# Kernel optimization log

Hardware: AMD Instinct MI355X
Metric: run time of the kernel (lower is better)

The kernel has to match this reference:

```python
import jax, jax.numpy as jnp
import numpy as np

B, S, L, H, DH, D = 16, 512, 12, 12, 64, 768
M = L + 1  # embed + L mlp outputs


def setup_inputs() -> dict:
    key = jax.random.key(0)
    ks = jax.random.split(key, 8)
    return {
        "mlp_stack": jax.random.normal(ks[0], (B, S, M, D), jnp.float32),
        "attn_stack": jax.random.normal(ks[1], (B, S, L, H, DH), jnp.float32),
        "mlp_mask": jax.random.uniform(ks[2], (B, M), jnp.float32),
        "attn_mask": jax.random.uniform(ks[3], (B, L, H), jnp.float32),
        "modal_mlp": jax.random.normal(ks[4], (M, D), jnp.float32),
        "modal_attention": jax.random.normal(ks[5], (L, H, D), jnp.float32),
        "W_O": jax.random.normal(ks[6], (L, H, DH, D), jnp.float32) * 0.02,
        "post_bias": jax.random.normal(ks[7], (L, D), jnp.float32) * 0.02,
    }


def reference(mlp_stack, attn_stack, mlp_mask, attn_mask, modal_mlp,
              modal_attention, W_O, post_bias):
    # pruning_edge_mlp_hook_all_tokens at layer_no = n_layers (final hook path),
    # cache_compressed_attn=True, ablation_backward=False, non-parallel inference.
    # masked edge-weighted sum over cached mlp outputs: [B,1,M,1]*[B,S,M,D] -> sum over M
    out = jnp.einsum('bm,bsmd->bsd', mlp_mask, mlp_stack)
    # ablation (modal) term for pruned mlp edges: broadcasts over pos
    out = out + jnp.einsum('bm,md->bd', 1.0 - mlp_mask, modal_mlp)[:, None, :]
    # masked attention-head edges, recombined through W_O:
    # ([B,1,P,H,1]*[B,S,P,H,K]) einsum [P,H,K,D] -> [B,S,D]
    attn_term = jnp.einsum('bph,bsphk,phkd->bsd', attn_mask, attn_stack, W_O)
    out = out + attn_term + post_bias.sum(axis=0)
    # ablation (modal) term for pruned attention edges, summed over layer & head
    out = out + jnp.einsum('bph,phd->bd', 1.0 - attn_mask, modal_attention)[:, None, :]
    return out
```

## Files before the change

### kernel.cpp

```cpp
#include <hip/hip_runtime.h>


#define D_ 768
#define K_ 9216
#define ROWS_ 8192

typedef __attribute__((ext_vector_type(8))) short short8;
typedef __attribute__((ext_vector_type(4))) float f32x4;

typedef unsigned int __attribute__((address_space(1))) gu32;
typedef unsigned int __attribute__((address_space(3))) lu32;

__device__ __forceinline__ void async_copy16(const void* g, void* l) {
    __builtin_amdgcn_global_load_lds((const gu32*)g, (lu32*)l, 16, 0, 0);
}

__device__ __forceinline__ unsigned short f2bf(float f) {
    union { float f; unsigned u; } a; a.f = f;
    unsigned r = a.u + 0x7FFF + ((a.u >> 16) & 1);
    return (unsigned short)(r >> 16);
}

__global__ __launch_bounds__(256) void bias_kernel(
    const float* __restrict__ mlp_mask, const float* __restrict__ attn_mask,
    const float* __restrict__ modal_mlp, const float* __restrict__ modal_att,
    const float* __restrict__ post_bias, float* __restrict__ bias) {
    int b = blockIdx.x;
    for (int d = threadIdx.x; d < D_; d += 256) {
        float acc = 0.f;
        #pragma unroll
        for (int p = 0; p < 12; ++p) acc += post_bias[p * D_ + d];
        #pragma unroll
        for (int m = 0; m < 13; ++m)
            acc += (1.f - mlp_mask[b * 13 + m]) * modal_mlp[m * D_ + d];
        for (int ph = 0; ph < 144; ++ph)
            acc += (1.f - attn_mask[b * 144 + ph]) * modal_att[ph * D_ + d];
        bias[b * D_ + d] = acc;
    }
}

__global__ __launch_bounds__(256) void transpose_wo(
    const float* __restrict__ W, unsigned short* __restrict__ Bt) {
    __shared__ float tile[32][33];
    int n0 = blockIdx.x * 32;
    int k0 = blockIdx.y * 32;
    int tx = threadIdx.x & 31, ty = threadIdx.x >> 5;
    #pragma unroll
    for (int i = 0; i < 4; ++i)
        tile[ty + 8 * i][tx] = W[(k0 + ty + 8 * i) * D_ + n0 + tx];
    __syncthreads();
    #pragma unroll
    for (int i = 0; i < 4; ++i)
        Bt[(n0 + ty + 8 * i) * K_ + k0 + tx] = f2bf(tile[tx][ty + 8 * i]);
}

__global__ __launch_bounds__(256) void conv_attn(
    const float* __restrict__ attn_stack, const float* __restrict__ attn_mask,
    unsigned short* __restrict__ A) {
    int bid = blockIdx.x;
    int row = bid / 9;
    int k = ((bid - row * 9) * 256 + threadIdx.x) * 4;
    int b = row >> 9;
    float w = attn_mask[b * 144 + (k >> 6)];
    int i = row * K_ + k;
    float4 v = *(const float4*)&attn_stack[i];
    ushort4 o;
    o.x = f2bf(v.x * w); o.y = f2bf(v.y * w);
    o.z = f2bf(v.z * w); o.w = f2bf(v.w * w);
    *(ushort4*)&A[i] = o;
}

__global__ __launch_bounds__(256) void mlp_kernel(
    const float* __restrict__ mlp_stack, const float* __restrict__ mlp_mask,
    const float* __restrict__ bias, float* __restrict__ out) {
    int i4 = (blockIdx.x * 256 + threadIdx.x) * 4;
    int row = i4 / D_;
    int d = i4 - row * D_;
    int b = row >> 9;
    float4 acc = *(const float4*)&bias[b * D_ + d];
    const float* base = mlp_stack + (long)row * 13 * D_ + d;
    #pragma unroll
    for (int m = 0; m < 13; ++m) {
        float w = mlp_mask[b * 13 + m];
        float4 v = *(const float4*)&base[m * D_];
        acc.x += w * v.x; acc.y += w * v.y;
        acc.z += w * v.z; acc.w += w * v.w;
    }
    *(float4*)&out[i4] = acc;
}

__global__ __launch_bounds__(256) void gemm_attn(
    const short* __restrict__ A, const short* __restrict__ Bt,
    float* __restrict__ out) {
    __shared__ __align__(16) short As[128 * 32];
    __shared__ __align__(16) short Bs[128 * 32];

    const int tid = threadIdx.x;
    const int wave = tid >> 6, lane = tid & 63;
    const int row0 = blockIdx.x * 128;
    const int col0 = blockIdx.y * 128;
    const int wr = (wave >> 1) * 64;
    const int wc = (wave & 1) * 64;

    f32x4 acc[4][4] = {};

    const int rc = lane >> 2;
    const int x = lane & 3;
    const int g = x ^ ((rc >> 1) & 3);

    int a_off[2], b_off[2], lds_off[2];
    #pragma unroll
    for (int j = 0; j < 2; ++j) {
        int c = wave * 2 + j;
        a_off[j] = (row0 + c * 16 + rc) * K_ + g * 8;
        b_off[j] = (col0 + c * 16 + rc) * K_ + g * 8;
        lds_off[j] = c * 1024;
    }

    const int fr = lane & 15;
    const int q = lane >> 4;
    const int pos = q ^ ((fr >> 1) & 3);

    for (int k0 = 0; k0 < K_; k0 += 32) {
        __syncthreads();
        #pragma unroll
        for (int j = 0; j < 2; ++j) {
            async_copy16(A + a_off[j] + k0, (char*)As + lds_off[j]);
            async_copy16(Bt + b_off[j] + k0, (char*)Bs + lds_off[j]);
        }
        __syncthreads();

        short8 af[4], bf[4];
        #pragma unroll
        for (int i = 0; i < 4; ++i) {
            af[i] = *(const short8*)&As[(wr + i * 16 + fr) * 32 + pos * 8];
            bf[i] = *(const short8*)&Bs[(wc + i * 16 + fr) * 32 + pos * 8];
        }
        #pragma unroll
        for (int i = 0; i < 4; ++i)
            #pragma unroll
            for (int j = 0; j < 4; ++j)
                acc[i][j] = __builtin_amdgcn_mfma_f32_16x16x32_bf16(
                    af[i], bf[j], acc[i][j], 0, 0, 0);
    }

    #pragma unroll
    for (int i = 0; i < 4; ++i) {
        int m = row0 + wr + i * 16 + q * 4;
        #pragma unroll
        for (int j = 0; j < 4; ++j) {
            int n = col0 + wc + j * 16 + fr;
            float* p = out + m * D_ + n;
            #pragma unroll
            for (int r = 0; r < 4; ++r)
                p[r * D_] += acc[i][j][r];
        }
    }
}

extern "C" void kernel_launch(void* const* d_in, const int* in_sizes, int n_in,
                              void* d_out, int out_size, void* d_ws, size_t ws_size,
                              hipStream_t stream) {
    const float* mlp_stack  = (const float*)d_in[0];
    const float* attn_stack = (const float*)d_in[1];
    const float* mlp_mask   = (const float*)d_in[2];
    const float* attn_mask  = (const float*)d_in[3];
    const float* modal_mlp  = (const float*)d_in[4];
    const float* modal_att  = (const float*)d_in[5];
    const float* W_O        = (const float*)d_in[6];
    const float* post_bias  = (const float*)d_in[7];
    float* out = (float*)d_out;

    char* ws = (char*)d_ws;
    unsigned short* Abf = (unsigned short*)ws;
    unsigned short* Btb = (unsigned short*)(ws + 150994944);
    float* bias = (float*)(ws + 150994944 + 14155776);

    bias_kernel<<<16, 256, 0, stream>>>(mlp_mask, attn_mask, modal_mlp,
                                        modal_att, post_bias, bias);
    transpose_wo<<<dim3(24, 288), 256, 0, stream>>>(W_O, Btb);
    conv_attn<<<73728, 256, 0, stream>>>(attn_stack, attn_mask, Abf);
    mlp_kernel<<<6144, 256, 0, stream>>>(mlp_stack, mlp_mask, bias, out);
    gemm_attn<<<dim3(64, 6), 256, 0, stream>>>((const short*)Abf, (const short*)Btb, out);
}
```

Baseline: 898.7 us.

## Split-K the attention GEMM with atomic accumulation and widen conversion kernels

The bf16 attention GEMM is split four ways along K, growing the grid from 384 to 1536 blocks so more of the 256 CUs are busy. Partial tiles are combined into the output with float atomicAdd. The conversion kernel now handles 8 elements per thread with 16-byte stores, and the bias kernel is spread over more blocks. The cost is atomic write traffic to the output and a summation order that can differ from run to run.

```diff
diff --git a/kernel.cpp b/kernel.cpp
--- a/kernel.cpp
+++ b/kernel.cpp
@@ -4,8 +4,11 @@
 #define D_ 768
 #define K_ 9216
 #define ROWS_ 8192
+#define SPLITS 4
+#define KSPLIT (K_ / SPLITS)
 
 typedef __attribute__((ext_vector_type(8))) short short8;
+typedef __attribute__((ext_vector_type(8))) unsigned short ushort8;
 typedef __attribute__((ext_vector_type(4))) float f32x4;
 
 typedef unsigned int __attribute__((address_space(1))) gu32;
@@ -26,17 +29,17 @@
     const float* __restrict__ modal_mlp, const float* __restrict__ modal_att,
     const float* __restrict__ post_bias, float* __restrict__ bias) {
     int b = blockIdx.x;
-    for (int d = threadIdx.x; d < D_; d += 256) {
-        float acc = 0.f;
-        #pragma unroll
-        for (int p = 0; p < 12; ++p) acc += post_bias[p * D_ + d];
-        #pragma unroll
-        for (int m = 0; m < 13; ++m)
-            acc += (1.f - mlp_mask[b * 13 + m]) * modal_mlp[m * D_ + d];
-        for (int ph = 0; ph < 144; ++ph)
-            acc += (1.f - attn_mask[b * 144 + ph]) * modal_att[ph * D_ + d];
-        bias[b * D_ + d] = acc;
-    }
+    int d = blockIdx.y * 256 + threadIdx.x;
+    float acc = 0.f;
+    #pragma unroll
+    for (int p = 0; p < 12; ++p) acc += post_bias[p * D_ + d];
+    #pragma unroll
+    for (int m = 0; m < 13; ++m)
+        acc += (1.f - mlp_mask[b * 13 + m]) * modal_mlp[m * D_ + d];
+    #pragma unroll 16
+    for (int ph = 0; ph < 144; ++ph)
+        acc += (1.f - attn_mask[b * 144 + ph]) * modal_att[ph * D_ + d];
+    bias[b * D_ + d] = acc;
 }
 
 __global__ __launch_bounds__(256) void transpose_wo(
@@ -57,17 +60,19 @@
 __global__ __launch_bounds__(256) void conv_attn(
     const float* __restrict__ attn_stack, const float* __restrict__ attn_mask,
     unsigned short* __restrict__ A) {
-    int bid = blockIdx.x;
-    int row = bid / 9;
-    int k = ((bid - row * 9) * 256 + threadIdx.x) * 4;
+    int i = (blockIdx.x * 256 + threadIdx.x) * 8;
+    int row = i / K_;
+    int k = i - row * K_;
     int b = row >> 9;
     float w = attn_mask[b * 144 + (k >> 6)];
-    int i = row * K_ + k;
-    float4 v = *(const float4*)&attn_stack[i];
-    ushort4 o;
-    o.x = f2bf(v.x * w); o.y = f2bf(v.y * w);
-    o.z = f2bf(v.z * w); o.w = f2bf(v.w * w);
-    *(ushort4*)&A[i] = o;
+    float4 v0 = *(const float4*)&attn_stack[i];
+    float4 v1 = *(const float4*)&attn_stack[i + 4];
+    ushort8 o;
+    o[0] = f2bf(v0.x * w); o[1] = f2bf(v0.y * w);
+    o[2] = f2bf(v0.z * w); o[3] = f2bf(v0.w * w);
+    o[4] = f2bf(v1.x * w); o[5] = f2bf(v1.y * w);
+    o[6] = f2bf(v1.z * w); o[7] = f2bf(v1.w * w);
+    *(ushort8*)&A[i] = o;
 }
 
 __global__ __launch_bounds__(256) void mlp_kernel(
@@ -99,6 +104,7 @@
     const int wave = tid >> 6, lane = tid & 63;
     const int row0 = blockIdx.x * 128;
     const int col0 = blockIdx.y * 128;
+    const int kStart = blockIdx.z * KSPLIT;
     const int wr = (wave >> 1) * 64;
     const int wc = (wave & 1) * 64;
 
@@ -112,8 +118,8 @@
     #pragma unroll
     for (int j = 0; j < 2; ++j) {
         int c = wave * 2 + j;
-        a_off[j] = (row0 + c * 16 + rc) * K_ + g * 8;
-        b_off[j] = (col0 + c * 16 + rc) * K_ + g * 8;
+        a_off[j] = (row0 + c * 16 + rc) * K_ + g * 8 + kStart;
+        b_off[j] = (col0 + c * 16 + rc) * K_ + g * 8 + kStart;
         lds_off[j] = c * 1024;
     }
 
@@ -121,7 +127,7 @@
     const int q = lane >> 4;
     const int pos = q ^ ((fr >> 1) & 3);
 
-    for (int k0 = 0; k0 < K_; k0 += 32) {
+    for (int k0 = 0; k0 < KSPLIT; k0 += 32) {
         __syncthreads();
         #pragma unroll
         for (int j = 0; j < 2; ++j) {
@@ -153,7 +159,7 @@
             float* p = out + m * D_ + n;
             #pragma unroll
             for (int r = 0; r < 4; ++r)
-                p[r * D_] += acc[i][j][r];
+                atomicAdd(p + r * D_, acc[i][j][r]);
         }
     }
 }
@@ -176,10 +182,11 @@
     unsigned short* Btb = (unsigned short*)(ws + 150994944);
     float* bias = (float*)(ws + 150994944 + 14155776);
 
-    bias_kernel<<<16, 256, 0, stream>>>(mlp_mask, attn_mask, modal_mlp,
-                                        modal_att, post_bias, bias);
+    bias_kernel<<<dim3(16, 3), 256, 0, stream>>>(mlp_mask, attn_mask, modal_mlp,
+                                                 modal_att, post_bias, bias);
     transpose_wo<<<dim3(24, 288), 256, 0, stream>>>(W_O, Btb);
-    conv_attn<<<73728, 256, 0, stream>>>(attn_stack, attn_mask, Abf);
+    conv_attn<<<36864, 256, 0, stream>>>(attn_stack, attn_mask, Abf);
     mlp_kernel<<<6144, 256, 0, stream>>>(mlp_stack, mlp_mask, bias, out);
-    gemm_attn<<<dim3(64, 6), 256, 0, stream>>>((const short*)Abf, (const short*)Btb, out);
+    gemm_attn<<<dim3(64, 6, SPLITS), 256, 0, stream>>>((const short*)Abf,
+                                                       (const short*)Btb, out);
 }
```

New measurement: 893.4 us. Within noise of the previous version (-0.6%).
